# Kernel tuning notes

Hardware: AMD Instinct MI355X
Metric: run time of the kernel (lower is better)

## Reference

```python
import jax, jax.numpy as jnp
import numpy as np

NUM_CLASSES = 80
AFS = 1024          # actors_features_size
OFS = 2048          # objects_features_size
NHEADS = 4
NHID = AFS // NHEADS + 4 // NHEADS   # 257
D = AFS + 4                           # 1028
ALPHA = 0.2                           # LeakyReLU slope
N_ACT, N_OBJ = 512, 3584


def _gat(x, adj_mask, W, a):
    # x: [N, D]; W: [H, D, NHID]; a: [H, 2*NHID]; adj_mask: [N, N] bool
    Wh = jnp.einsum('nf,hfd->hnd', x, W)                      # [H, N, NHID]
    f1 = jnp.einsum('hnd,hd->hn', Wh, a[:, :NHID])            # src score
    f2 = jnp.einsum('hnd,hd->hn', Wh, a[:, NHID:])            # dst score
    e = f1[:, :, None] + f2[:, None, :]                       # [H, N, N]
    e = jnp.where(e > 0, e, ALPHA * e)                        # LeakyReLU
    e = jnp.where(adj_mask[None], e, jnp.asarray(-9e15, e.dtype))
    att = jax.nn.softmax(e, axis=-1)                          # [H, N, N]
    h = jnp.einsum('hnm,hmd->hnd', att, Wh)                   # [H, N, NHID]
    h = jax.nn.elu(h)
    return jnp.transpose(h, (1, 0, 2)).reshape(x.shape[0], NHEADS * NHID)


def _ln(x, g, b):
    m = jnp.mean(x, axis=-1, keepdims=True)
    v = jnp.mean((x - m) ** 2, axis=-1, keepdims=True)
    return (x - m) * jax.lax.rsqrt(v + 1e-5) * g + b


def setup_inputs() -> dict:
    key = jax.random.key(0)
    ks = jax.random.split(key, 24)
    d = {
        'actors_features': jax.random.normal(ks[0], (N_ACT, 1024, 4, 7, 7), jnp.float32),
        'actors_labels': jax.random.uniform(ks[1], (N_ACT, NUM_CLASSES), jnp.float32),
        'actors_boxes': jax.random.uniform(ks[2], (N_ACT, 4), jnp.float32),
        'objects_features': jax.random.normal(ks[3], (N_OBJ, OFS), jnp.float32),
        'objects_boxes': jax.random.uniform(ks[4], (N_OBJ, 4), jnp.float32),
        'adj': jax.random.randint(ks[5], (N_ACT + N_OBJ, N_ACT + N_OBJ), 0, 2, jnp.int32),
    }
    s = lambda k, shp, fan: jax.random.normal(k, shp, jnp.float32) * (1.0 / np.sqrt(fan))
    d['obj_W'] = s(ks[6], (OFS, AFS), OFS)
    d['obj_b'] = jnp.zeros((AFS,), jnp.float32)
    d['gat1_W'] = s(ks[7], (NHEADS, D, NHID), D)
    d['gat1_a'] = s(ks[8], (NHEADS, 2 * NHID), 2 * NHID)
    d['gat_fc_W'] = s(ks[9], (D, D), D)
    d['gat_fc_b'] = jnp.zeros((D,), jnp.float32)
    d['ln1_g'] = jnp.ones((D,), jnp.float32)
    d['ln1_b'] = jnp.zeros((D,), jnp.float32)
    d['gat2_W'] = s(ks[10], (NHEADS, D, NHID), D)
    d['gat2_a'] = s(ks[11], (NHEADS, 2 * NHID), 2 * NHID)
    d['gat_fc2_W'] = s(ks[12], (D, D), D)
    d['gat_fc2_b'] = jnp.zeros((D,), jnp.float32)
    d['ln2_g'] = jnp.ones((D,), jnp.float32)
    d['ln2_b'] = jnp.zeros((D,), jnp.float32)
    d['logits_W'] = s(ks[13], (D, NUM_CLASSES), D)
    d['logits_b'] = jnp.zeros((NUM_CLASSES,), jnp.float32)
    return d


def reference(actors_features, actors_labels, actors_boxes, objects_features,
              objects_boxes, adj, obj_W, obj_b, gat1_W, gat1_a, gat_fc_W,
              gat_fc_b, ln1_g, ln1_b, gat2_W, gat2_a, gat_fc2_W, gat_fc2_b,
              ln2_g, ln2_b, logits_W, logits_b):
    ab, ob = actors_boxes, objects_boxes
    a_geo = jnp.stack([ab[:, 3] - ab[:, 1], ab[:, 2] - ab[:, 0],
                       (ab[:, 2] - ab[:, 0]) / 2 + ab[:, 0],
                       (ab[:, 3] - ab[:, 1]) / 2 + ab[:, 1]], axis=1)
    o_geo = jnp.stack([ob[:, 3] - ob[:, 1], ob[:, 2] - ob[:, 0],
                       (ob[:, 2] - ob[:, 0]) / 2 + ob[:, 0],
                       (ob[:, 3] - ob[:, 1]) / 2 + ob[:, 1]], axis=1)
    # torch.no_grad mean-pool over T,H,W -> [N, C]
    af = jax.lax.stop_gradient(jnp.mean(actors_features, axis=(2, 3, 4)))
    af = jnp.concatenate([af, a_geo], axis=1)                 # [Na, D]
    of = jax.nn.relu(objects_features @ obj_W + obj_b)        # reducer (OFS>AFS)
    of = jnp.concatenate([of, o_geo], axis=1)                 # [No, D]
    x = jnp.concatenate([af, of], axis=0)                     # [N, D]
    mask = adj > 0
    g = _gat(x, mask, gat1_W, gat1_a)
    x = _ln(x + g @ gat_fc_W + gat_fc_b, ln1_g, ln1_b)
    g = _gat(x, mask, gat2_W, gat2_a)
    x = _ln(x + g @ gat_fc2_W + gat_fc2_b, ln2_g, ln2_b)
    logits = x[:af.shape[0]] @ logits_W + logits_b            # [Na, C]
    y = actors_labels
    loss = jnp.mean(jnp.clip(logits, 0, None) - logits * y
                    + jnp.log1p(jnp.exp(-jnp.abs(logits))))
    return jax.nn.sigmoid(logits), loss
```

## Files before the change

### kernel.cpp

```cpp
#include <hip/hip_runtime.h>
#include <cstdint>

#define NACT 512
#define NOBJ 3584
#define NTOT 4096
#define DCOLS 1028
#define NHID_ 257
#define OFSZ 2048
#define KPAD 1056
#define NPADH 384
#define NPADFC 1152

typedef float f32x4 __attribute__((ext_vector_type(4)));
typedef short short8v __attribute__((ext_vector_type(8)));
typedef short short4v __attribute__((ext_vector_type(4)));

static const size_t OFF_X0    = 0;
static const size_t OFF_T     = 4210688;
static const size_t OFF_F1    = 8421376;
static const size_t OFF_F2    = 8437760;
static const size_t OFF_RMAX  = 8454144;
static const size_t OFF_RDEN  = 8470528;
static const size_t OFF_LOSSP = 8486912;
static const size_t OFF_MASK  = 8487424;
static const size_t OFF_XB    = 9011712;
static const size_t OFF_GB    = 11174400;
static const size_t OFF_OBJWT = 13337088;
static const size_t OFF_GATWT = 14385664;
static const size_t OFF_FCWT  = 16007680;
static const size_t OFF_WHT   = 17224192;

__device__ __forceinline__ short f2bf(float x) {
    unsigned u = __float_as_uint(x);
    u += 0x7fffu + ((u >> 16) & 1u);
    return (short)(u >> 16);
}
__device__ __forceinline__ int swz(int row, int chunk) {
    return row * 64 + (((chunk ^ ((row >> 1) & 3))) << 4);
}

__global__ void k_geo(const float* __restrict__ ab, const float* __restrict__ ob,
                      float* __restrict__ X) {
    int n = blockIdx.x * blockDim.x + threadIdx.x;
    if (n >= NTOT) return;
    const float* b = (n < NACT) ? &ab[n * 4] : &ob[(n - NACT) * 4];
    float x0 = b[0], y0 = b[1], x1 = b[2], y1 = b[3];
    float* o = &X[(size_t)n * DCOLS + 1024];
    o[0] = y1 - y0;
    o[1] = x1 - x0;
    o[2] = (x1 - x0) * 0.5f + x0;
    o[3] = (y1 - y0) * 0.5f + y0;
}

__global__ __launch_bounds__(256) void k_meanpool(const float* __restrict__ af,
                                                  float* __restrict__ X) {
    int w = blockIdx.x * 4 + (threadIdx.x >> 6);
    int lane = threadIdx.x & 63;
    const float* src = af + (size_t)w * 196;
    float s = src[lane] + src[lane + 64] + src[lane + 128];
    if (lane < 4) s += src[192 + lane];
    #pragma unroll
    for (int off = 32; off; off >>= 1) s += __shfl_down(s, off);
    if (lane == 0) {
        int n = w >> 10, c = w & 1023;
        X[(size_t)n * DCOLS + c] = s * (1.0f / 196.0f);
    }
}

__global__ __launch_bounds__(256) void k_packmask(const int* __restrict__ adj,
                                                  unsigned long long* __restrict__ mb) {
    int w = blockIdx.x * 4 + (threadIdx.x >> 6);
    int lane = threadIdx.x & 63;
    int v = adj[(size_t)w * 64 + lane];
    unsigned long long m = __ballot(v > 0);
    if (lane == 0) mb[w] = m;
}

__global__ __launch_bounds__(256) void k_transpW(const float* __restrict__ W, int K, int N,
                                                 short* __restrict__ Wt, int Kpad, int Npad) {
    __shared__ float Ws[32][33];
    int k0 = blockIdx.x * 32, n0 = blockIdx.y * 32;
    int t = threadIdx.x;
    #pragma unroll
    for (int i = 0; i < 4; ++i) {
        int j = t + i * 256;
        int r = j >> 5, c = j & 31;
        float v = 0.f;
        if (k0 + r < K && n0 + c < N) v = W[(size_t)(k0 + r) * N + n0 + c];
        Ws[r][c] = v;
    }
    __syncthreads();
    #pragma unroll
    for (int i = 0; i < 4; ++i) {
        int j = t + i * 256;
        int n = j >> 5, k = j & 31;
        Wt[(size_t)(n0 + n) * Kpad + k0 + k] = f2bf(Ws[k][n]);
    }
}

__global__ __launch_bounds__(256) void k_convX(const float* __restrict__ X,
                                               short* __restrict__ Xb) {
    int i = blockIdx.x * 256 + threadIdx.x;
    int n = i / 132, g = i % 132;
    int c0 = g * 8;
    short8v o;
    if (c0 + 8 <= DCOLS) {
        float4 v0 = *reinterpret_cast<const float4*>(&X[(size_t)n * DCOLS + c0]);
        float4 v1 = *reinterpret_cast<const float4*>(&X[(size_t)n * DCOLS + c0 + 4]);
        o[0]=f2bf(v0.x); o[1]=f2bf(v0.y); o[2]=f2bf(v0.z); o[3]=f2bf(v0.w);
        o[4]=f2bf(v1.x); o[5]=f2bf(v1.y); o[6]=f2bf(v1.z); o[7]=f2bf(v1.w);
    } else {
        #pragma unroll
        for (int j = 0; j < 8; ++j)
            o[j] = (c0 + j < DCOLS) ? f2bf(X[(size_t)n * DCOLS + c0 + j]) : (short)0;
    }
    *reinterpret_cast<short8v*>(&Xb[(size_t)n * KPAD + c0]) = o;
}

template <int MODE>
__global__ __launch_bounds__(256, 2) void k_mm(
    const void* __restrict__ Aptr, int lda,
    const short* __restrict__ Bt, int ldb,
    void* __restrict__ Cptr, int ldc,
    const float* __restrict__ bias,
    const float* __restrict__ resid, int ldr,
    float* __restrict__ F1, float* __restrict__ F2,
    const float* __restrict__ AV,
    int nk, int Nvalid) {
    __shared__ char sm[16384];
    const int t = threadIdx.x;
    const int m0 = blockIdx.x * 128;
    const int n0 = blockIdx.y * 128;
    const int z = blockIdx.z;

    short* Cwh = nullptr;
    float* Cf  = nullptr;
    if constexpr (MODE == 1) {
        Bt += (size_t)z * (NPADH * KPAD);
        Cwh = (short*)Cptr + (size_t)z * ((size_t)NPADH * NTOT);
        AV += z * (2 * NHID_);
        F1 += z * NTOT; F2 += z * NTOT;
    } else {
        Cf = (float*)Cptr;
    }

    const int ar = t >> 1, acp = t & 1;
    const int wv = t >> 6, lane = t & 63, lr = lane & 15, lk = lane >> 4;
    const int wr = wv >> 1, wc = wv & 1;
    int aoff[4], boff[4];
    #pragma unroll
    for (int i = 0; i < 4; ++i) aoff[i] = swz(64 * wr + 16 * i + lr, lk);
    #pragma unroll
    for (int j = 0; j < 4; ++j) boff[j] = 8192 + swz(64 * wc + 16 * j + lr, lk);

    f32x4 acc[4][4];
    #pragma unroll
    for (int i = 0; i < 4; ++i)
        #pragma unroll
        for (int j = 0; j < 4; ++j) acc[i][j] = (f32x4){0.f, 0.f, 0.f, 0.f};

    for (int kt = 0; kt < nk; ++kt) {
        const int k0 = kt * 32;
        if constexpr (MODE == 0) {
            const float* ap = (const float*)Aptr + (size_t)(m0 + ar) * lda + k0 + acp * 16;
            float4 u0 = *reinterpret_cast<const float4*>(ap);
            float4 u1 = *reinterpret_cast<const float4*>(ap + 4);
            float4 u2 = *reinterpret_cast<const float4*>(ap + 8);
            float4 u3 = *reinterpret_cast<const float4*>(ap + 12);
            short8v s0, s1;
            s0[0]=f2bf(u0.x); s0[1]=f2bf(u0.y); s0[2]=f2bf(u0.z); s0[3]=f2bf(u0.w);
            s0[4]=f2bf(u1.x); s0[5]=f2bf(u1.y); s0[6]=f2bf(u1.z); s0[7]=f2bf(u1.w);
            s1[0]=f2bf(u2.x); s1[1]=f2bf(u2.y); s1[2]=f2bf(u2.z); s1[3]=f2bf(u2.w);
            s1[4]=f2bf(u3.x); s1[5]=f2bf(u3.y); s1[6]=f2bf(u3.z); s1[7]=f2bf(u3.w);
            *reinterpret_cast<short8v*>(sm + swz(ar, 2 * acp)) = s0;
            *reinterpret_cast<short8v*>(sm + swz(ar, 2 * acp + 1)) = s1;
        } else {
            const short* ap = (const short*)Aptr + (size_t)(m0 + ar) * lda + k0 + acp * 16;
            short8v v0 = *reinterpret_cast<const short8v*>(ap);
            short8v v1 = *reinterpret_cast<const short8v*>(ap + 8);
            *reinterpret_cast<short8v*>(sm + swz(ar, 2 * acp)) = v0;
            *reinterpret_cast<short8v*>(sm + swz(ar, 2 * acp + 1)) = v1;
        }
        {
            const short* bp = Bt + (size_t)(n0 + ar) * ldb + k0 + acp * 16;
            short8v v0 = *reinterpret_cast<const short8v*>(bp);
            short8v v1 = *reinterpret_cast<const short8v*>(bp + 8);
            *reinterpret_cast<short8v*>(sm + 8192 + swz(ar, 2 * acp)) = v0;
            *reinterpret_cast<short8v*>(sm + 8192 + swz(ar, 2 * acp + 1)) = v1;
        }
        __syncthreads();
        short8v a[4], b[4];
        #pragma unroll
        for (int i = 0; i < 4; ++i) a[i] = *reinterpret_cast<short8v*>(sm + aoff[i]);
        #pragma unroll
        for (int j = 0; j < 4; ++j) b[j] = *reinterpret_cast<short8v*>(sm + boff[j]);
        #pragma unroll
        for (int i = 0; i < 4; ++i)
            #pragma unroll
            for (int j = 0; j < 4; ++j)
                acc[i][j] = __builtin_amdgcn_mfma_f32_16x16x32_bf16(a[i], b[j], acc[i][j], 0, 0, 0);
        __syncthreads();
    }

    const int mb0 = m0 + 64 * wr + 4 * lk;
    const int cb0 = n0 + 64 * wc + lr;
    if constexpr (MODE == 0 || MODE == 3) {
        #pragma unroll
        for (int i = 0; i < 4; ++i)
            #pragma unroll
            for (int j = 0; j < 4; ++j) {
                int c = cb0 + 16 * j;
                if (c < Nvalid) {
                    #pragma unroll
                    for (int rr = 0; rr < 4; ++rr) {
                        int m = mb0 + 16 * i + rr;
                        float v = acc[i][j][rr] + bias[c];
                        if constexpr (MODE == 0) v = fmaxf(v, 0.f);
                        if constexpr (MODE == 3) v += resid[(size_t)m * ldr + c];
                        Cf[(size_t)m * ldc + c] = v;
                    }
                }
            }
    } else {
        float la1[4], la2[4];
        #pragma unroll
        for (int j = 0; j < 4; ++j) {
            int d = cb0 + 16 * j;
            la1[j] = (d < NHID_) ? AV[d] : 0.f;
            la2[j] = (d < NHID_) ? AV[NHID_ + d] : 0.f;
        }
        #pragma unroll
        for (int i = 0; i < 4; ++i) {
            #pragma unroll
            for (int j = 0; j < 4; ++j) {
                int d = cb0 + 16 * j;
                short4v o;
                o[0] = f2bf(acc[i][j][0]); o[1] = f2bf(acc[i][j][1]);
                o[2] = f2bf(acc[i][j][2]); o[3] = f2bf(acc[i][j][3]);
                *reinterpret_cast<short4v*>(&Cwh[(size_t)d * NTOT + mb0 + 16 * i]) = o;
            }
            #pragma unroll
            for (int rr = 0; rr < 4; ++rr) {
                float s1 = 0.f, s2 = 0.f;
                #pragma unroll
                for (int j = 0; j < 4; ++j) {
                    s1 += acc[i][j][rr] * la1[j];
                    s2 += acc[i][j][rr] * la2[j];
                }
                #pragma unroll
                for (int mk = 1; mk < 16; mk <<= 1) {
                    s1 += __shfl_xor(s1, mk);
                    s2 += __shfl_xor(s2, mk);
                }
                if (lr == 0) {
                    int m = mb0 + 16 * i + rr;
                    atomicAdd(&F1[m], s1);
                    atomicAdd(&F2[m], s2);
                }
            }
        }
    }
}

__global__ __launch_bounds__(256, 1) void k_pv(
    const short* __restrict__ WHT,
    const float* __restrict__ F1, const float* __restrict__ F2,
    const float* __restrict__ RMAX, const float* __restrict__ RDEN,
    const unsigned long long* __restrict__ MB,
    short* __restrict__ Gb) {
    __shared__ char sm[28672];
    const int t = threadIdx.x;
    const int m0 = blockIdx.x * 64;
    const int h = blockIdx.z;
    const short* WhH = WHT + (size_t)h * ((size_t)NPADH * NTOT);
    const float* F1h = F1 + h * NTOT;
    const float* F2h = F2 + h * NTOT;
    const int gcol = h * NHID_;

    const int pr = t >> 2, pq = t & 3;
    const int n = m0 + pr;
    const float f1n = F1h[n];
    const float rmx = RMAX[h * NTOT + n];
    const float psc = 1.0f / RDEN[h * NTOT + n];
    const unsigned long long* mrow = MB + (size_t)n * 64;

    const int vr = t >> 1, vcp = t & 1;

    const int wv = t >> 6, lane = t & 63, lr = lane & 15, lk = lane >> 4;
    int aoff[4], boff[6];
    #pragma unroll
    for (int i = 0; i < 4; ++i) aoff[i] = swz(16 * i + lr, lk);
    #pragma unroll
    for (int j = 0; j < 6; ++j) boff[j] = 4096 + swz(96 * wv + 16 * j + lr, lk);

    f32x4 acc[4][6];
    #pragma unroll
    for (int i = 0; i < 4; ++i)
        #pragma unroll
        for (int j = 0; j < 6; ++j) acc[i][j] = (f32x4){0.f, 0.f, 0.f, 0.f};

    for (int kt = 0; kt < NTOT / 32; ++kt) {
        const int k0 = kt * 32;
        {
            const int mk = k0 + pq * 8;
            unsigned long long wbits = mrow[k0 >> 6] >> ((k0 & 63) + pq * 8);
            float4 q0 = *reinterpret_cast<const float4*>(F2h + mk);
            float4 q1 = *reinterpret_cast<const float4*>(F2h + mk + 4);
            float fv[8] = {q0.x, q0.y, q0.z, q0.w, q1.x, q1.y, q1.z, q1.w};
            short8v o;
            #pragma unroll
            for (int j = 0; j < 8; ++j) {
                float e = f1n + fv[j];
                e = e > 0.f ? e : 0.2f * e;
                float p = ((wbits >> j) & 1ULL) ? __expf(e - rmx) * psc : 0.f;
                o[j] = f2bf(p);
            }
            *reinterpret_cast<short8v*>(sm + swz(pr, pq)) = o;
        }
        #pragma unroll
        for (int rep = 0; rep < 3; ++rep) {
            int row = vr + rep * 128;
            const short* vp = WhH + (size_t)row * NTOT + k0 + vcp * 16;
            short8v v0 = *reinterpret_cast<const short8v*>(vp);
            short8v v1 = *reinterpret_cast<const short8v*>(vp + 8);
            *reinterpret_cast<short8v*>(sm + 4096 + swz(row, 2 * vcp)) = v0;
            *reinterpret_cast<short8v*>(sm + 4096 + swz(row, 2 * vcp + 1)) = v1;
        }
        __syncthreads();
        short8v a[4], b[6];
        #pragma unroll
        for (int i = 0; i < 4; ++i) a[i] = *reinterpret_cast<short8v*>(sm + aoff[i]);
        #pragma unroll
        for (int j = 0; j < 6; ++j) b[j] = *reinterpret_cast<short8v*>(sm + boff[j]);
        #pragma unroll
        for (int i = 0; i < 4; ++i)
            #pragma unroll
            for (int j = 0; j < 6; ++j)
                acc[i][j] = __builtin_amdgcn_mfma_f32_16x16x32_bf16(a[i], b[j], acc[i][j], 0, 0, 0);
        __syncthreads();
    }

    #pragma unroll
    for (int j = 0; j < 6; ++j) {
        int d = 96 * wv + 16 * j + lr;
        if (d < NHID_) {
            #pragma unroll
            for (int i = 0; i < 4; ++i)
                #pragma unroll
                for (int rr = 0; rr < 4; ++rr) {
                    int m = m0 + 16 * i + 4 * lk + rr;
                    float v = acc[i][j][rr];
                    v = v > 0.f ? v : expm1f(v);
                    Gb[(size_t)m * KPAD + gcol + d] = f2bf(v);
                }
        }
    }
}

__global__ __launch_bounds__(256) void k_rowstat(const float* __restrict__ F1,
                                                 const float* __restrict__ F2,
                                                 const unsigned long long* __restrict__ mb,
                                                 float* __restrict__ RMAX, float* __restrict__ RDEN) {
    __shared__ float f2s[NTOT];
    __shared__ unsigned long long mw[4][64];
    int h = blockIdx.y;
    const float4* src = reinterpret_cast<const float4*>(F2 + (size_t)h * NTOT);
    float4* dst = reinterpret_cast<float4*>(f2s);
    for (int i = threadIdx.x; i < NTOT / 4; i += 256) dst[i] = src[i];
    int wv = threadIdx.x >> 6, lane = threadIdx.x & 63;
    int n = blockIdx.x * 4 + wv;
    mw[wv][lane] = mb[(size_t)n * 64 + lane];
    __syncthreads();
    float f1n = F1[(size_t)h * NTOT + n];
    float rm = -1e30f, rs = 0.f;
    for (int b = 0; b < 64; ++b) {
        unsigned long long wb = mw[wv][b];
        if ((wb >> lane) & 1ULL) {
            float e = f1n + f2s[b * 64 + lane];
            e = e > 0.f ? e : 0.2f * e;
            if (e > rm) { rs *= __expf(rm - e); rm = e; }
            rs += __expf(e - rm);
        }
    }
    #pragma unroll
    for (int off = 32; off; off >>= 1) {
        float m2 = __shfl_down(rm, off), s2 = __shfl_down(rs, off);
        float nm = fmaxf(rm, m2);
        rs = rs * __expf(rm - nm) + s2 * __expf(m2 - nm);
        rm = nm;
    }
    if (lane == 0) {
        if (rs == 0.f) rs = 1.f;
        RMAX[(size_t)h * NTOT + n] = rm;
        RDEN[(size_t)h * NTOT + n] = rs;
    }
}

__global__ __launch_bounds__(256) void k_ln(const float* __restrict__ T,
                                            const float* __restrict__ g,
                                            const float* __restrict__ b,
                                            float* __restrict__ O) {
    int n = blockIdx.x;
    const float* row = T + (size_t)n * DCOLS;
    float s = 0.f, q = 0.f;
    for (int i = threadIdx.x; i < DCOLS / 4; i += 256) {
        float4 v = *reinterpret_cast<const float4*>(&row[i * 4]);
        s += v.x + v.y + v.z + v.w;
        q += v.x * v.x + v.y * v.y + v.z * v.z + v.w * v.w;
    }
    __shared__ float ls[2][4];
    int lane = threadIdx.x & 63, wv = threadIdx.x >> 6;
    #pragma unroll
    for (int off = 32; off; off >>= 1) {
        s += __shfl_down(s, off);
        q += __shfl_down(q, off);
    }
    if (lane == 0) { ls[0][wv] = s; ls[1][wv] = q; }
    __syncthreads();
    s = ls[0][0] + ls[0][1] + ls[0][2] + ls[0][3];
    q = ls[1][0] + ls[1][1] + ls[1][2] + ls[1][3];
    float mean = s * (1.0f / DCOLS);
    float var = q * (1.0f / DCOLS) - mean * mean;
    float rstd = rsqrtf(var + 1e-5f);
    float* orow = O + (size_t)n * DCOLS;
    for (int i = threadIdx.x; i < DCOLS; i += 256)
        orow[i] = (row[i] - mean) * rstd * g[i] + b[i];
}

__global__ __launch_bounds__(128) void k_logits(const float* __restrict__ X,
                                                const float* __restrict__ W,
                                                const float* __restrict__ bias,
                                                const float* __restrict__ Y,
                                                float* __restrict__ out,
                                                float* __restrict__ lossp) {
    __shared__ float xs[DCOLS];
    int n = blockIdx.x;
    for (int i = threadIdx.x; i < DCOLS / 4; i += 128)
        *reinterpret_cast<float4*>(&xs[i * 4]) =
            *reinterpret_cast<const float4*>(&X[(size_t)n * DCOLS + i * 4]);
    __syncthreads();
    float loss = 0.f;
    int c = threadIdx.x;
    if (c < 80) {
        float acc = bias[c];
        for (int k = 0; k < DCOLS; ++k) acc += xs[k] * W[k * 80 + c];
        out[n * 80 + c] = 1.0f / (1.0f + expf(-acc));
        float y = Y[n * 80 + c];
        loss = fmaxf(acc, 0.f) - acc * y + log1pf(expf(-fabsf(acc)));
    }
    __shared__ float lr[2];
    int lane = threadIdx.x & 63, wv = threadIdx.x >> 6;
    #pragma unroll
    for (int off = 32; off; off >>= 1) loss += __shfl_down(loss, off);
    if (lane == 0) lr[wv] = loss;
    __syncthreads();
    if (threadIdx.x == 0) lossp[n] = lr[0] + lr[1];
}

__global__ __launch_bounds__(256) void k_lossfin(const float* __restrict__ lossp,
                                                 float* __restrict__ out) {
    float s = 0.f;
    for (int i = threadIdx.x; i < NACT; i += 256) s += lossp[i];
    #pragma unroll
    for (int off = 32; off; off >>= 1) s += __shfl_down(s, off);
    __shared__ float lr[4];
    int lane = threadIdx.x & 63, wv = threadIdx.x >> 6;
    if (lane == 0) lr[wv] = s;
    __syncthreads();
    if (threadIdx.x == 0) out[NACT * 80] = (lr[0] + lr[1] + lr[2] + lr[3]) / (float)(NACT * 80);
}

extern "C" void kernel_launch(void* const* d_in, const int* in_sizes, int n_in,
                              void* d_out, int out_size, void* d_ws, size_t ws_size,
                              hipStream_t stream) {
    const float* actors_features  = (const float*)d_in[0];
    const float* actors_labels    = (const float*)d_in[1];
    const float* actors_boxes     = (const float*)d_in[2];
    const float* objects_features = (const float*)d_in[3];
    const float* objects_boxes    = (const float*)d_in[4];
    const int*   adj              = (const int*)d_in[5];
    const float* obj_W    = (const float*)d_in[6];
    const float* obj_b    = (const float*)d_in[7];
    const float* gatW[2]  = {(const float*)d_in[8],  (const float*)d_in[14]};
    const float* gatA[2]  = {(const float*)d_in[9],  (const float*)d_in[15]};
    const float* fcW[2]   = {(const float*)d_in[10], (const float*)d_in[16]};
    const float* fcB[2]   = {(const float*)d_in[11], (const float*)d_in[17]};
    const float* lnG[2]   = {(const float*)d_in[12], (const float*)d_in[18]};
    const float* lnB[2]   = {(const float*)d_in[13], (const float*)d_in[19]};
    const float* logits_W = (const float*)d_in[20];
    const float* logits_b = (const float*)d_in[21];
    float* out = (float*)d_out;

    float* ws   = (float*)d_ws;
    float* X0   = ws + OFF_X0;
    float* T    = ws + OFF_T;
    float* F1   = ws + OFF_F1;
    float* F2   = ws + OFF_F2;
    float* RMAX = ws + OFF_RMAX;
    float* RDEN = ws + OFF_RDEN;
    float* LOSSP= ws + OFF_LOSSP;
    unsigned long long* MASK = (unsigned long long*)(ws + OFF_MASK);
    short* Xb    = (short*)(ws + OFF_XB);
    short* Gb    = (short*)(ws + OFF_GB);
    short* objWt = (short*)(ws + OFF_OBJWT);
    short* gatWt = (short*)(ws + OFF_GATWT);
    short* fcWt  = (short*)(ws + OFF_FCWT);
    short* WHT   = (short*)(ws + OFF_WHT);

    hipMemsetAsync(F1, 0, 2 * 4 * NTOT * sizeof(float), stream);
    hipMemsetAsync(Gb, 0, (size_t)NTOT * KPAD * 2, stream);

    k_geo<<<(NTOT + 255) / 256, 256, 0, stream>>>(actors_boxes, objects_boxes, X0);
    k_meanpool<<<(NACT * 1024) / 4, 256, 0, stream>>>(actors_features, X0);
    k_packmask<<<(NTOT * 64) / 4, 256, 0, stream>>>(adj, MASK);

    k_transpW<<<dim3(64, 32), 256, 0, stream>>>(obj_W, OFSZ, 1024, objWt, OFSZ, 1024);
    for (int L = 0; L < 2; ++L) {
        for (int h = 0; h < 4; ++h)
            k_transpW<<<dim3(33, 12), 256, 0, stream>>>(
                gatW[L] + (size_t)h * DCOLS * NHID_, DCOLS, NHID_,
                gatWt + (size_t)(L * 4 + h) * NPADH * KPAD, KPAD, NPADH);
        k_transpW<<<dim3(33, 36), 256, 0, stream>>>(
            fcW[L], DCOLS, DCOLS, fcWt + (size_t)L * NPADFC * KPAD, KPAD, NPADFC);
    }

    k_mm<0><<<dim3(NOBJ / 128, 1024 / 128, 1), 256, 0, stream>>>(
        objects_features, OFSZ, objWt, OFSZ, X0 + (size_t)NACT * DCOLS, DCOLS,
        obj_b, nullptr, 0, nullptr, nullptr, nullptr,
        OFSZ / 32, 1024);

    k_convX<<<(NTOT * 132) / 256, 256, 0, stream>>>(X0, Xb);

    const float* xin = X0;
    for (int L = 0; L < 2; ++L) {
        if (L == 1) {
            hipMemsetAsync(F1, 0, 2 * 4 * NTOT * sizeof(float), stream);
            k_convX<<<(NTOT * 132) / 256, 256, 0, stream>>>(T, Xb);
        }
        k_mm<1><<<dim3(NTOT / 128, NPADH / 128, 4), 256, 0, stream>>>(
            Xb, KPAD, gatWt + (size_t)L * 4 * NPADH * KPAD, KPAD, WHT, 0,
            nullptr, nullptr, 0, F1, F2, gatA[L],
            KPAD / 32, NHID_);
        k_rowstat<<<dim3(NTOT / 4, 4), 256, 0, stream>>>(F1, F2, MASK, RMAX, RDEN);
        k_pv<<<dim3(NTOT / 64, 1, 4), 256, 0, stream>>>(
            WHT, F1, F2, RMAX, RDEN, MASK, Gb);
        k_mm<3><<<dim3(NTOT / 128, NPADFC / 128, 1), 256, 0, stream>>>(
            Gb, KPAD, fcWt + (size_t)L * NPADFC * KPAD, KPAD, T, DCOLS,
            fcB[L], xin, DCOLS, nullptr, nullptr, nullptr,
            KPAD / 32, DCOLS);
        k_ln<<<NTOT, 256, 0, stream>>>(T, lnG[L], lnB[L], T);
        xin = T;
    }
    k_logits<<<NACT, 128, 0, stream>>>(T, logits_W, logits_b, actors_labels, out, LOSSP);
    k_lossfin<<<1, 256, 0, stream>>>(LOSSP, out);
}
```

Baseline: 1.558 ms.

## Double-buffer GEMMs with direct global-to-LDS loads, fuse bf16 conversions, shrink head padding

The GEMM and PV kernels now double-buffer their LDS tiles and fill them with global_load_lds, so the next tile's load overlaps the current tile's MFMA work. Object features are converted to bf16 up front, and the bf16 copies of X are written directly by geo, meanpool, obj-GEMM and layernorm, which removes the separate convX passes. Head padding drops from 384 to 320 and the heads are folded into the grid's y dimension. The PV kernel gets an XCD-aware block mapping and two blocks per CU. The costs are extra LDS per block, an added memset and conversion pass, and more register pressure.

Result: faster. 1.432 ms (-8.1%).

```diff
diff --git a/kernel.cpp b/kernel.cpp
--- a/kernel.cpp
+++ b/kernel.cpp
@@ -8,7 +8,8 @@
 #define NHID_ 257
 #define OFSZ 2048
 #define KPAD 1056
-#define NPADH 384
+#define NPADH 320
+#define NWH   1280
 #define NPADFC 1152
 
 typedef float f32x4 __attribute__((ext_vector_type(4)));
@@ -25,10 +26,11 @@
 static const size_t OFF_MASK  = 8487424;
 static const size_t OFF_XB    = 9011712;
 static const size_t OFF_GB    = 11174400;
-static const size_t OFF_OBJWT = 13337088;
-static const size_t OFF_GATWT = 14385664;
-static const size_t OFF_FCWT  = 16007680;
-static const size_t OFF_WHT   = 17224192;
+static const size_t OFF_OFB   = 13337088;
+static const size_t OFF_OBJWT = 17007104;
+static const size_t OFF_GATWT = 18055680;
+static const size_t OFF_FCWT  = 19407360;
+static const size_t OFF_WHT   = 20623872;
 
 __device__ __forceinline__ short f2bf(float x) {
     unsigned u = __float_as_uint(x);
@@ -38,22 +40,29 @@
 __device__ __forceinline__ int swz(int row, int chunk) {
     return row * 64 + (((chunk ^ ((row >> 1) & 3))) << 4);
 }
+__device__ __forceinline__ void gload16(const void* g, void* l) {
+    __builtin_amdgcn_global_load_lds(
+        (const __attribute__((address_space(1))) unsigned int*)g,
+        (__attribute__((address_space(3))) unsigned int*)l, 16, 0, 0);
+}
 
 __global__ void k_geo(const float* __restrict__ ab, const float* __restrict__ ob,
-                      float* __restrict__ X) {
+                      float* __restrict__ X, short* __restrict__ Xb) {
     int n = blockIdx.x * blockDim.x + threadIdx.x;
     if (n >= NTOT) return;
     const float* b = (n < NACT) ? &ab[n * 4] : &ob[(n - NACT) * 4];
     float x0 = b[0], y0 = b[1], x1 = b[2], y1 = b[3];
+    float g0 = y1 - y0, g1 = x1 - x0;
+    float g2 = (x1 - x0) * 0.5f + x0, g3 = (y1 - y0) * 0.5f + y0;
     float* o = &X[(size_t)n * DCOLS + 1024];
-    o[0] = y1 - y0;
-    o[1] = x1 - x0;
-    o[2] = (x1 - x0) * 0.5f + x0;
-    o[3] = (y1 - y0) * 0.5f + y0;
+    o[0] = g0; o[1] = g1; o[2] = g2; o[3] = g3;
+    short* ob2 = &Xb[(size_t)n * KPAD + 1024];
+    ob2[0] = f2bf(g0); ob2[1] = f2bf(g1); ob2[2] = f2bf(g2); ob2[3] = f2bf(g3);
 }
 
 __global__ __launch_bounds__(256) void k_meanpool(const float* __restrict__ af,
-                                                  float* __restrict__ X) {
+                                                  float* __restrict__ X,
+                                                  short* __restrict__ Xb) {
     int w = blockIdx.x * 4 + (threadIdx.x >> 6);
     int lane = threadIdx.x & 63;
     const float* src = af + (size_t)w * 196;
@@ -63,7 +72,9 @@
     for (int off = 32; off; off >>= 1) s += __shfl_down(s, off);
     if (lane == 0) {
         int n = w >> 10, c = w & 1023;
-        X[(size_t)n * DCOLS + c] = s * (1.0f / 196.0f);
+        float v = s * (1.0f / 196.0f);
+        X[(size_t)n * DCOLS + c] = v;
+        Xb[(size_t)n * KPAD + c] = f2bf(v);
     }
 }
 
@@ -76,8 +87,20 @@
     if (lane == 0) mb[w] = m;
 }
 
+__global__ __launch_bounds__(256) void k_convF(const float* __restrict__ src,
+                                               short* __restrict__ dst, int n8) {
+    int i = blockIdx.x * 256 + threadIdx.x;
+    if (i >= n8) return;
+    float4 a = *reinterpret_cast<const float4*>(src + (size_t)i * 8);
+    float4 b = *reinterpret_cast<const float4*>(src + (size_t)i * 8 + 4);
+    short8v o;
+    o[0]=f2bf(a.x); o[1]=f2bf(a.y); o[2]=f2bf(a.z); o[3]=f2bf(a.w);
+    o[4]=f2bf(b.x); o[5]=f2bf(b.y); o[6]=f2bf(b.z); o[7]=f2bf(b.w);
+    *reinterpret_cast<short8v*>(dst + (size_t)i * 8) = o;
+}
+
 __global__ __launch_bounds__(256) void k_transpW(const float* __restrict__ W, int K, int N,
-                                                 short* __restrict__ Wt, int Kpad, int Npad) {
+                                                 short* __restrict__ Wt, int Kpad) {
     __shared__ float Ws[32][33];
     int k0 = blockIdx.x * 32, n0 = blockIdx.y * 32;
     int t = threadIdx.x;
@@ -98,55 +121,24 @@
     }
 }
 
-__global__ __launch_bounds__(256) void k_convX(const float* __restrict__ X,
-                                               short* __restrict__ Xb) {
-    int i = blockIdx.x * 256 + threadIdx.x;
-    int n = i / 132, g = i % 132;
-    int c0 = g * 8;
-    short8v o;
-    if (c0 + 8 <= DCOLS) {
-        float4 v0 = *reinterpret_cast<const float4*>(&X[(size_t)n * DCOLS + c0]);
-        float4 v1 = *reinterpret_cast<const float4*>(&X[(size_t)n * DCOLS + c0 + 4]);
-        o[0]=f2bf(v0.x); o[1]=f2bf(v0.y); o[2]=f2bf(v0.z); o[3]=f2bf(v0.w);
-        o[4]=f2bf(v1.x); o[5]=f2bf(v1.y); o[6]=f2bf(v1.z); o[7]=f2bf(v1.w);
-    } else {
-        #pragma unroll
-        for (int j = 0; j < 8; ++j)
-            o[j] = (c0 + j < DCOLS) ? f2bf(X[(size_t)n * DCOLS + c0 + j]) : (short)0;
-    }
-    *reinterpret_cast<short8v*>(&Xb[(size_t)n * KPAD + c0]) = o;
-}
-
 template <int MODE>
 __global__ __launch_bounds__(256, 2) void k_mm(
-    const void* __restrict__ Aptr, int lda,
+    const short* __restrict__ Ab, int lda,
     const short* __restrict__ Bt, int ldb,
     void* __restrict__ Cptr, int ldc,
     const float* __restrict__ bias,
     const float* __restrict__ resid, int ldr,
     float* __restrict__ F1, float* __restrict__ F2,
     const float* __restrict__ AV,
+    short* __restrict__ Cbf,
     int nk, int Nvalid) {
-    __shared__ char sm[16384];
+    __shared__ char sm[32768];
     const int t = threadIdx.x;
     const int m0 = blockIdx.x * 128;
     const int n0 = blockIdx.y * 128;
-    const int z = blockIdx.z;
-
-    short* Cwh = nullptr;
-    float* Cf  = nullptr;
-    if constexpr (MODE == 1) {
-        Bt += (size_t)z * (NPADH * KPAD);
-        Cwh = (short*)Cptr + (size_t)z * ((size_t)NPADH * NTOT);
-        AV += z * (2 * NHID_);
-        F1 += z * NTOT; F2 += z * NTOT;
-    } else {
-        Cf = (float*)Cptr;
-    }
-
-    const int ar = t >> 1, acp = t & 1;
     const int wv = t >> 6, lane = t & 63, lr = lane & 15, lk = lane >> 4;
     const int wr = wv >> 1, wc = wv & 1;
+
     int aoff[4], boff[4];
     #pragma unroll
     for (int i = 0; i < 4; ++i) aoff[i] = swz(64 * wr + 16 * i + lr, lk);
@@ -159,85 +151,82 @@
         #pragma unroll
         for (int j = 0; j < 4; ++j) acc[i][j] = (f32x4){0.f, 0.f, 0.f, 0.f};
 
+    auto stage = [&](int p, int k0) {
+        char* base = sm + p * 16384;
+        #pragma unroll
+        for (int c = 0; c < 2; ++c) {
+            int slot = 2 * wv + c;
+            int row = slot * 16 + (lane >> 2);
+            int gch = (lane & 3) ^ ((row >> 1) & 3);
+            gload16(Ab + (size_t)(m0 + row) * lda + k0 + gch * 8, base + slot * 1024);
+            gload16(Bt + (size_t)(n0 + row) * ldb + k0 + gch * 8, base + 8192 + slot * 1024);
+        }
+    };
+
+    stage(0, 0);
+    __syncthreads();
+    int p = 0;
     for (int kt = 0; kt < nk; ++kt) {
-        const int k0 = kt * 32;
-        if constexpr (MODE == 0) {
-            const float* ap = (const float*)Aptr + (size_t)(m0 + ar) * lda + k0 + acp * 16;
-            float4 u0 = *reinterpret_cast<const float4*>(ap);
-            float4 u1 = *reinterpret_cast<const float4*>(ap + 4);
-            float4 u2 = *reinterpret_cast<const float4*>(ap + 8);
-            float4 u3 = *reinterpret_cast<const float4*>(ap + 12);
-            short8v s0, s1;
-            s0[0]=f2bf(u0.x); s0[1]=f2bf(u0.y); s0[2]=f2bf(u0.z); s0[3]=f2bf(u0.w);
-            s0[4]=f2bf(u1.x); s0[5]=f2bf(u1.y); s0[6]=f2bf(u1.z); s0[7]=f2bf(u1.w);
-            s1[0]=f2bf(u2.x); s1[1]=f2bf(u2.y); s1[2]=f2bf(u2.z); s1[3]=f2bf(u2.w);
-            s1[4]=f2bf(u3.x); s1[5]=f2bf(u3.y); s1[6]=f2bf(u3.z); s1[7]=f2bf(u3.w);
-            *reinterpret_cast<short8v*>(sm + swz(ar, 2 * acp)) = s0;
-            *reinterpret_cast<short8v*>(sm + swz(ar, 2 * acp + 1)) = s1;
-        } else {
-            const short* ap = (const short*)Aptr + (size_t)(m0 + ar) * lda + k0 + acp * 16;
-            short8v v0 = *reinterpret_cast<const short8v*>(ap);
-            short8v v1 = *reinterpret_cast<const short8v*>(ap + 8);
-            *reinterpret_cast<short8v*>(sm + swz(ar, 2 * acp)) = v0;
-            *reinterpret_cast<short8v*>(sm + swz(ar, 2 * acp + 1)) = v1;
-        }
-        {
-            const short* bp = Bt + (size_t)(n0 + ar) * ldb + k0 + acp * 16;
-            short8v v0 = *reinterpret_cast<const short8v*>(bp);
-            short8v v1 = *reinterpret_cast<const short8v*>(bp + 8);
-            *reinterpret_cast<short8v*>(sm + 8192 + swz(ar, 2 * acp)) = v0;
-            *reinterpret_cast<short8v*>(sm + 8192 + swz(ar, 2 * acp + 1)) = v1;
-        }
-        __syncthreads();
+        if (kt + 1 < nk) stage(p ^ 1, (kt + 1) * 32);
+        const char* cb = sm + p * 16384;
         short8v a[4], b[4];
         #pragma unroll
-        for (int i = 0; i < 4; ++i) a[i] = *reinterpret_cast<short8v*>(sm + aoff[i]);
-        #pragma unroll
-        for (int j = 0; j < 4; ++j) b[j] = *reinterpret_cast<short8v*>(sm + boff[j]);
+        for (int i = 0; i < 4; ++i) a[i] = *reinterpret_cast<const short8v*>(cb + aoff[i]);
+        #pragma unroll
+        for (int j = 0; j < 4; ++j) b[j] = *reinterpret_cast<const short8v*>(cb + boff[j]);
         #pragma unroll
         for (int i = 0; i < 4; ++i)
             #pragma unroll
             for (int j = 0; j < 4; ++j)
                 acc[i][j] = __builtin_amdgcn_mfma_f32_16x16x32_bf16(a[i], b[j], acc[i][j], 0, 0, 0);
         __syncthreads();
+        p ^= 1;
     }
 
     const int mb0 = m0 + 64 * wr + 4 * lk;
-    const int cb0 = n0 + 64 * wc + lr;
     if constexpr (MODE == 0 || MODE == 3) {
+        float* Cf = (float*)Cptr;
         #pragma unroll
         for (int i = 0; i < 4; ++i)
             #pragma unroll
             for (int j = 0; j < 4; ++j) {
-                int c = cb0 + 16 * j;
+                int c = n0 + 64 * wc + 16 * j + lr;
                 if (c < Nvalid) {
                     #pragma unroll
                     for (int rr = 0; rr < 4; ++rr) {
                         int m = mb0 + 16 * i + rr;
                         float v = acc[i][j][rr] + bias[c];
-                        if constexpr (MODE == 0) v = fmaxf(v, 0.f);
+                        if constexpr (MODE == 0) v = fmaxf(v, 0.0f);
                         if constexpr (MODE == 3) v += resid[(size_t)m * ldr + c];
                         Cf[(size_t)m * ldc + c] = v;
+                        if constexpr (MODE == 0) Cbf[(size_t)m * KPAD + c] = f2bf(v);
                     }
                 }
             }
     } else {
+        const int cwbase = n0 + 64 * wc;
+        const int h = cwbase / NPADH;
+        const int dwbase = cwbase - h * NPADH;
+        const float* AVh = AV + h * (2 * NHID_);
+        float* F1h = F1 + h * NTOT;
+        float* F2h = F2 + h * NTOT;
+        short* CwhH = (short*)Cptr + (size_t)h * ((size_t)NPADH * NTOT);
         float la1[4], la2[4];
         #pragma unroll
         for (int j = 0; j < 4; ++j) {
-            int d = cb0 + 16 * j;
-            la1[j] = (d < NHID_) ? AV[d] : 0.f;
-            la2[j] = (d < NHID_) ? AV[NHID_ + d] : 0.f;
+            int d = dwbase + 16 * j + lr;
+            la1[j] = (d < NHID_) ? AVh[d] : 0.f;
+            la2[j] = (d < NHID_) ? AVh[NHID_ + d] : 0.f;
         }
         #pragma unroll
         for (int i = 0; i < 4; ++i) {
             #pragma unroll
             for (int j = 0; j < 4; ++j) {
-                int d = cb0 + 16 * j;
+                int d = dwbase + 16 * j + lr;
                 short4v o;
                 o[0] = f2bf(acc[i][j][0]); o[1] = f2bf(acc[i][j][1]);
                 o[2] = f2bf(acc[i][j][2]); o[3] = f2bf(acc[i][j][3]);
-                *reinterpret_cast<short4v*>(&Cwh[(size_t)d * NTOT + mb0 + 16 * i]) = o;
+                *reinterpret_cast<short4v*>(&CwhH[(size_t)d * NTOT + mb0 + 16 * i]) = o;
             }
             #pragma unroll
             for (int rr = 0; rr < 4; ++rr) {
@@ -254,95 +243,104 @@
                 }
                 if (lr == 0) {
                     int m = mb0 + 16 * i + rr;
-                    atomicAdd(&F1[m], s1);
-                    atomicAdd(&F2[m], s2);
+                    atomicAdd(&F1h[m], s1);
+                    atomicAdd(&F2h[m], s2);
                 }
             }
         }
     }
 }
 
-__global__ __launch_bounds__(256, 1) void k_pv(
+__global__ __launch_bounds__(256, 2) void k_pv(
     const short* __restrict__ WHT,
     const float* __restrict__ F1, const float* __restrict__ F2,
     const float* __restrict__ RMAX, const float* __restrict__ RDEN,
     const unsigned long long* __restrict__ MB,
     short* __restrict__ Gb) {
-    __shared__ char sm[28672];
+    __shared__ char sm[49152];
     const int t = threadIdx.x;
-    const int m0 = blockIdx.x * 64;
-    const int h = blockIdx.z;
+    const int i0 = blockIdx.x;
+    const int xcd = i0 & 7, slot = i0 >> 3;
+    const int h = xcd >> 1;
+    const int m0 = (slot * 2 + (xcd & 1)) * 64;
     const short* WhH = WHT + (size_t)h * ((size_t)NPADH * NTOT);
-    const float* F1h = F1 + h * NTOT;
     const float* F2h = F2 + h * NTOT;
     const int gcol = h * NHID_;
 
     const int pr = t >> 2, pq = t & 3;
     const int n = m0 + pr;
-    const float f1n = F1h[n];
+    const float f1n = F1[h * NTOT + n];
     const float rmx = RMAX[h * NTOT + n];
     const float psc = 1.0f / RDEN[h * NTOT + n];
     const unsigned long long* mrow = MB + (size_t)n * 64;
 
-    const int vr = t >> 1, vcp = t & 1;
-
     const int wv = t >> 6, lane = t & 63, lr = lane & 15, lk = lane >> 4;
-    int aoff[4], boff[6];
+    int aoff[4], boff[5];
     #pragma unroll
     for (int i = 0; i < 4; ++i) aoff[i] = swz(16 * i + lr, lk);
     #pragma unroll
-    for (int j = 0; j < 6; ++j) boff[j] = 4096 + swz(96 * wv + 16 * j + lr, lk);
-
-    f32x4 acc[4][6];
+    for (int j = 0; j < 5; ++j) boff[j] = 4096 + swz(80 * wv + 16 * j + lr, lk);
+
+    f32x4 acc[4][5];
     #pragma unroll
     for (int i = 0; i < 4; ++i)
         #pragma unroll
-        for (int j = 0; j < 6; ++j) acc[i][j] = (f32x4){0.f, 0.f, 0.f, 0.f};
-
+        for (int j = 0; j < 5; ++j) acc[i][j] = (f32x4){0.f, 0.f, 0.f, 0.f};
+
+    auto stageV = [&](int p, int k0) {
+        char* vb = sm + p * 24576 + 4096;
+        #pragma unroll
+        for (int c = 0; c < 5; ++c) {
+            int slot2 = 5 * wv + c;
+            int row = slot2 * 16 + (lane >> 2);
+            int gch = (lane & 3) ^ ((row >> 1) & 3);
+            gload16(WhH + (size_t)row * NTOT + k0 + gch * 8, vb + slot2 * 1024);
+        }
+    };
+    auto pgen = [&](int p, int k0) {
+        const int mk = k0 + pq * 8;
+        unsigned long long wbits = mrow[k0 >> 6] >> ((k0 & 63) + pq * 8);
+        float4 q0 = *reinterpret_cast<const float4*>(F2h + mk);
+        float4 q1 = *reinterpret_cast<const float4*>(F2h + mk + 4);
+        float fv[8] = {q0.x, q0.y, q0.z, q0.w, q1.x, q1.y, q1.z, q1.w};
+        short8v o;
+        #pragma unroll
+        for (int j = 0; j < 8; ++j) {
+            float e = f1n + fv[j];
+            e = e > 0.f ? e : 0.2f * e;
+            float pvv = ((wbits >> j) & 1ULL) ? __expf(e - rmx) * psc : 0.f;
+            o[j] = f2bf(pvv);
+        }
+        *reinterpret_cast<short8v*>(sm + p * 24576 + swz(pr, pq)) = o;
+    };
+
+    stageV(0, 0);
+    pgen(0, 0);
+    __syncthreads();
+    int p = 0;
     for (int kt = 0; kt < NTOT / 32; ++kt) {
-        const int k0 = kt * 32;
-        {
-            const int mk = k0 + pq * 8;
-            unsigned long long wbits = mrow[k0 >> 6] >> ((k0 & 63) + pq * 8);
-            float4 q0 = *reinterpret_cast<const float4*>(F2h + mk);
-            float4 q1 = *reinterpret_cast<const float4*>(F2h + mk + 4);
-            float fv[8] = {q0.x, q0.y, q0.z, q0.w, q1.x, q1.y, q1.z, q1.w};
-            short8v o;
-            #pragma unroll
-            for (int j = 0; j < 8; ++j) {
-                float e = f1n + fv[j];
-                e = e > 0.f ? e : 0.2f * e;
-                float p = ((wbits >> j) & 1ULL) ? __expf(e - rmx) * psc : 0.f;
-                o[j] = f2bf(p);
-            }
-            *reinterpret_cast<short8v*>(sm + swz(pr, pq)) = o;
-        }
-        #pragma unroll
-        for (int rep = 0; rep < 3; ++rep) {
-            int row = vr + rep * 128;
-            const short* vp = WhH + (size_t)row * NTOT + k0 + vcp * 16;
-            short8v v0 = *reinterpret_cast<const short8v*>(vp);
-            short8v v1 = *reinterpret_cast<const short8v*>(vp + 8);
-            *reinterpret_cast<short8v*>(sm + 4096 + swz(row, 2 * vcp)) = v0;
-            *reinterpret_cast<short8v*>(sm + 4096 + swz(row, 2 * vcp + 1)) = v1;
-        }
-        __syncthreads();
-        short8v a[4], b[6];
-        #pragma unroll
-        for (int i = 0; i < 4; ++i) a[i] = *reinterpret_cast<short8v*>(sm + aoff[i]);
-        #pragma unroll
-        for (int j = 0; j < 6; ++j) b[j] = *reinterpret_cast<short8v*>(sm + boff[j]);
+        if (kt + 1 < NTOT / 32) {
+            stageV(p ^ 1, (kt + 1) * 32);
+            pgen(p ^ 1, (kt + 1) * 32);
+        }
+        const char* cb = sm + p * 24576;
+        short8v a[4], b[5];
+        #pragma unroll
+        for (int i = 0; i < 4; ++i) a[i] = *reinterpret_cast<const short8v*>(cb + aoff[i]);
+        #pragma unroll
+        for (int j = 0; j < 5; ++j) b[j] = *reinterpret_cast<const short8v*>(cb + boff[j]);
         #pragma unroll
         for (int i = 0; i < 4; ++i)
             #pragma unroll
-            for (int j = 0; j < 6; ++j)
+            for (int j = 0; j < 5; ++j)
                 acc[i][j] = __builtin_amdgcn_mfma_f32_16x16x32_bf16(a[i], b[j], acc[i][j], 0, 0, 0);
         __syncthreads();
-    }
-
-    #pragma unroll
-    for (int j = 0; j < 6; ++j) {
-        int d = 96 * wv + 16 * j + lr;
+        p ^= 1;
+    }
+
+    #pragma unroll
+    for (int j = 0; j < 5; ++j) {
+        int d = 80 * wv + 16 * j + lr;
         if (d < NHID_) {
             #pragma unroll
             for (int i = 0; i < 4; ++i)
@@ -399,7 +397,8 @@
 __global__ __launch_bounds__(256) void k_ln(const float* __restrict__ T,
                                             const float* __restrict__ g,
                                             const float* __restrict__ b,
-                                            float* __restrict__ O) {
+                                            float* __restrict__ O,
+                                            short* __restrict__ xb) {
     int n = blockIdx.x;
     const float* row = T + (size_t)n * DCOLS;
     float s = 0.f, q = 0.f;
@@ -423,8 +422,11 @@
     float var = q * (1.0f / DCOLS) - mean * mean;
     float rstd = rsqrtf(var + 1e-5f);
     float* orow = O + (size_t)n * DCOLS;
-    for (int i = threadIdx.x; i < DCOLS; i += 256)
-        orow[i] = (row[i] - mean) * rstd * g[i] + b[i];
+    for (int i = threadIdx.x; i < DCOLS; i += 256) {
+        float v = (row[i] - mean) * rstd * g[i] + b[i];
+        orow[i] = v;
+        if (xb) xb[(size_t)n * KPAD + i] = f2bf(v);
+    }
 }
 
 __global__ __launch_bounds__(128) void k_logits(const float* __restrict__ X,
@@ -502,6 +504,7 @@
     unsigned long long* MASK = (unsigned long long*)(ws + OFF_MASK);
     short* Xb    = (short*)(ws + OFF_XB);
     short* Gb    = (short*)(ws + OFF_GB);
+    short* OFb   = (short*)(ws + OFF_OFB);
     short* objWt = (short*)(ws + OFF_OBJWT);
     short* gatWt = (short*)(ws + OFF_GATWT);
     short* fcWt  = (short*)(ws + OFF_FCWT);
@@ -509,46 +512,43 @@
 
     hipMemsetAsync(F1, 0, 2 * 4 * NTOT * sizeof(float), stream);
     hipMemsetAsync(Gb, 0, (size_t)NTOT * KPAD * 2, stream);
-
-    k_geo<<<(NTOT + 255) / 256, 256, 0, stream>>>(actors_boxes, objects_boxes, X0);
-    k_meanpool<<<(NACT * 1024) / 4, 256, 0, stream>>>(actors_features, X0);
+    hipMemsetAsync(Xb, 0, (size_t)NTOT * KPAD * 2, stream);
+
+    k_geo<<<(NTOT + 255) / 256, 256, 0, stream>>>(actors_boxes, objects_boxes, X0, Xb);
+    k_meanpool<<<(NACT * 1024) / 4, 256, 0, stream>>>(actors_features, X0, Xb);
     k_packmask<<<(NTOT * 64) / 4, 256, 0, stream>>>(adj, MASK);
-
-    k_transpW<<<dim3(64, 32), 256, 0, stream>>>(obj_W, OFSZ, 1024, objWt, OFSZ, 1024);
+    k_convF<<<(NOBJ * OFSZ / 8 + 255) / 256, 256, 0, stream>>>(objects_features, OFb, NOBJ * OFSZ / 8);
+
+    k_transpW<<<dim3(64, 32), 256, 0, stream>>>(obj_W, OFSZ, 1024, objWt, OFSZ);
     for (int L = 0; L < 2; ++L) {
         for (int h = 0; h < 4; ++h)
-            k_transpW<<<dim3(33, 12), 256, 0, stream>>>(
+            k_transpW<<<dim3(33, 10), 256, 0, stream>>>(
                 gatW[L] + (size_t)h * DCOLS * NHID_, DCOLS, NHID_,
-                gatWt + (size_t)(L * 4 + h) * NPADH * KPAD, KPAD, NPADH);
+                gatWt + (size_t)L * NWH * KPAD + (size_t)h * NPADH * KPAD, KPAD);
         k_transpW<<<dim3(33, 36), 256, 0, stream>>>(
-            fcW[L], DCOLS, DCOLS, fcWt + (size_t)L * NPADFC * KPAD, KPAD, NPADFC);
-    }
-
-    k_mm<0><<<dim3(NOBJ / 128, 1024 / 128, 1), 256, 0, stream>>>(
-        objects_features, OFSZ, objWt, OFSZ, X0 + (size_t)NACT * DCOLS, DCOLS,
+            fcW[L], DCOLS, DCOLS, fcWt + (size_t)L * NPADFC * KPAD, KPAD);
+    }
+
+    k_mm<0><<<dim3(NOBJ / 128, 1024 / 128), 256, 0, stream>>>(
+        OFb, OFSZ, objWt, OFSZ, X0 + (size_t)NACT * DCOLS, DCOLS,
         obj_b, nullptr, 0, nullptr, nullptr, nullptr,
-        OFSZ / 32, 1024);
-
-    k_convX<<<(NTOT * 132) / 256, 256, 0, stream>>>(X0, Xb);
+        Xb + (size_t)NACT * KPAD, OFSZ / 32, 1024);
 
     const float* xin = X0;
     for (int L = 0; L < 2; ++L) {
-        if (L == 1) {
+        if (L == 1)
             hipMemsetAsync(F1, 0, 2 * 4 * NTOT * sizeof(float), stream);
-            k_convX<<<(NTOT * 132) / 256, 256, 0, stream>>>(T, Xb);
-        }
-        k_mm<1><<<dim3(NTOT / 128, NPADH / 128, 4), 256, 0, stream>>>(
-            Xb, KPAD, gatWt + (size_t)L * 4 * NPADH * KPAD, KPAD, WHT, 0,
-            nullptr, nullptr, 0, F1, F2, gatA[L],
+        k_mm<1><<<dim3(NTOT / 128, NWH / 128), 256, 0, stream>>>(
+            Xb, KPAD, gatWt + (size_t)L * NWH * KPAD, KPAD, WHT, 0,
+            nullptr, nullptr, 0, F1, F2, gatA[L], nullptr,
             KPAD / 32, NHID_);
         k_rowstat<<<dim3(NTOT / 4, 4), 256, 0, stream>>>(F1, F2, MASK, RMAX, RDEN);
-        k_pv<<<dim3(NTOT / 64, 1, 4), 256, 0, stream>>>(
-            WHT, F1, F2, RMAX, RDEN, MASK, Gb);
-        k_mm<3><<<dim3(NTOT / 128, NPADFC / 128, 1), 256, 0, stream>>>(
+        k_pv<<<256, 256, 0, stream>>>(WHT, F1, F2, RMAX, RDEN, MASK, Gb);
+        k_mm<3><<<dim3(NTOT / 128, NPADFC / 128), 256, 0, stream>>>(
             Gb, KPAD, fcWt + (size_t)L * NPADFC * KPAD, KPAD, T, DCOLS,
-            fcB[L], xin, DCOLS, nullptr, nullptr, nullptr,
+            fcB[L], xin, DCOLS, nullptr, nullptr, nullptr, nullptr,
             KPAD / 32, DCOLS);
-        k_ln<<<NTOT, 256, 0, stream>>>(T, lnG[L], lnB[L], T);
+        k_ln<<<NTOT, 256, 0, stream>>>(T, lnG[L], lnB[L], T, (L == 0) ? Xb : nullptr);
         xin = T;
     }
     k_logits<<<NACT, 128, 0, stream>>>(T, logits_W, logits_b, actors_labels, out, LOSSP);
```
